# Performance work log

Measured on AMD Instinct MI355X. Metric: run time of the kernel, lower is better.

## Reference

```python
import jax, jax.numpy as jnp
import numpy as np

SIGMA_READ = 0.5
EPS = 1e-8

def setup_inputs() -> dict:
    key = jax.random.key(0)
    k1, k2, k3, k4, k5 = jax.random.split(key, 5)
    B, T, D = 2, 512, 128
    N, DV, DE = 100000, 256, 4
    q = jax.random.normal(k1, (B, T, D), dtype=jnp.float32)
    q = q / jnp.linalg.norm(q, axis=-1, keepdims=True)  # normalized queries
    K = jax.random.normal(k2, (N, D), dtype=jnp.float32)
    K = K / jnp.linalg.norm(K, axis=-1, keepdims=True)  # F.normalize(K, dim=-1)
    V = jax.random.normal(k3, (N, DV), dtype=jnp.float32)
    h = jax.random.uniform(k4, (N,), dtype=jnp.float32)  # intensities > 0
    e = jax.random.uniform(k5, (N, DE), dtype=jnp.float32)
    return {"queries": q, "K": K, "V": V, "h": h, "e": e, "top_k": 32}

def reference(queries, K, V, h, e, top_k):
    # similarities: [B, T, N]; all centers assumed active
    sim = jnp.einsum('btd,nd->btn', queries, K)
    dist_sq = 2.0 - 2.0 * sim
    rbf = jnp.exp(-dist_sq / (2.0 * SIGMA_READ ** 2))
    # top-k RBF weights and their center indices: [B, T, k]
    topk_w, topk_idx = jax.lax.top_k(rbf, top_k)
    h_topk = h[topk_idx]
    log_w = jnp.log(topk_w + EPS) + jnp.log(h_topk + EPS)
    weights = jax.nn.softmax(log_w, axis=-1)
    V_sel = V[topk_idx]  # [B, T, k, DV]
    e_sel = e[topk_idx]  # [B, T, k, DE]
    r_V = jnp.einsum('btk,btkv->btv', weights, V_sel)
    r_E = jnp.einsum('btk,btke->bte', weights, e_sel)
    return r_V, r_E, weights, topk_idx
```

## Files before the change

### kernel.cpp

```cpp
#include <hip/hip_runtime.h>
#include <math.h>


#define DDIM    128
#define MSAMPLE 12288
#define NBINS   256
#define TOPK    32
#define NQTOT   1024
#define NGRP    128
#define BCAP    24
#define EPSM    0.012f
#define SORTN   1024
#define FINEN   256
#define QSH     17
#define QMASK   0x1FFFFu
#define QMARGIN 200u

typedef __attribute__((ext_vector_type(8))) short short8;
typedef __attribute__((ext_vector_type(4))) float f32x4;

__device__ inline unsigned short f2bf(float f) {
    unsigned u = __builtin_bit_cast(unsigned, f);
    return (unsigned short)((u + 0x7FFFu + ((u >> 16) & 1u)) >> 16);
}

__global__ __launch_bounds__(256)
void convert_kernel(const float* __restrict__ Qg, const float* __restrict__ Kg,
                    unsigned short* __restrict__ Qbf, unsigned short* __restrict__ Kbf,
                    int nq8, int nk8)
{
    int total = nq8 + nk8;
    for (int i = blockIdx.x * 256 + threadIdx.x; i < total; i += gridDim.x * 256) {
        const float* s; unsigned short* d; int j;
        if (i < nq8) { s = Qg; d = Qbf; j = i; }
        else         { s = Kg; d = Kbf; j = i - nq8; }
        float4 a = *reinterpret_cast<const float4*>(s + (size_t)j * 8);
        float4 b = *reinterpret_cast<const float4*>(s + (size_t)j * 8 + 4);
        short8 o;
        o[0] = (short)f2bf(a.x); o[1] = (short)f2bf(a.y);
        o[2] = (short)f2bf(a.z); o[3] = (short)f2bf(a.w);
        o[4] = (short)f2bf(b.x); o[5] = (short)f2bf(b.y);
        o[6] = (short)f2bf(b.z); o[7] = (short)f2bf(b.w);
        *reinterpret_cast<short8*>(d + (size_t)j * 8) = o;
    }
}

template<int MODE>
__global__ __launch_bounds__(256)
void gemm_pass(const unsigned short* __restrict__ Qb, const unsigned short* __restrict__ Kb,
               int N, unsigned char* __restrict__ binsU8,
               const float* __restrict__ thr,
               int* __restrict__ cnt2, unsigned int* __restrict__ buckets)
{
    __shared__ __align__(16) unsigned char Bs[2][64 * 256];
    __shared__ int off_l[64];
    const int tid   = threadIdx.x;
    const int lane  = tid & 63;
    const int w     = tid >> 6;
    const int wr    = (w >> 1) * 32;
    const int wc    = (w & 1) * 32;
    const int lr    = lane & 15;
    const int lk    = lane >> 4;
    const int g     = blockIdx.x;
    const int qbase = blockIdx.y * 64;

    int t0, tcnt;
    if (MODE == 0) { t0 = g; tcnt = 1; }
    else { t0 = g * 12 + min(g, 27); tcnt = 12 + (g < 27 ? 1 : 0); }

    if (MODE == 1)
        for (int i = tid; i < 64; i += 256) off_l[i] = 0;

#define STAGE(buf, tile) do {                                                  \
    const int cbase_ = (tile) * 64;                                            \
    _Pragma("unroll")                                                          \
    for (int it = 0; it < 4; ++it) {                                           \
        int flat = it * 256 + tid;                                             \
        int r_ = flat >> 4, cc_ = flat & 15;                                   \
        int row_ = cbase_ + r_;                                                \
        if (MODE == 1 && row_ >= N) row_ = N - 1;   \
        const unsigned short* src_ = Kb + (size_t)row_ * DDIM                  \
                                        + ((cc_ ^ (r_ & 15)) * 8);             \
        unsigned char* dst_ = &Bs[buf][(size_t)(it * 256 + (tid & ~63)) * 16]; \
        __builtin_amdgcn_global_load_lds(                                      \
            (const __attribute__((address_space(1))) unsigned int*)src_,       \
            (__attribute__((address_space(3))) unsigned int*)dst_, 16, 0, 0);  \
    }                                                                          \
} while (0)

    short8 af[2][4];
    #pragma unroll
    for (int fm = 0; fm < 2; ++fm)
        #pragma unroll
        for (int ks = 0; ks < 4; ++ks)
            af[fm][ks] = *reinterpret_cast<const short8*>(
                Qb + (size_t)(qbase + wr + fm * 16 + lr) * DDIM + (ks * 4 + lk) * 8);

    float thrv[2][4];
    if (MODE == 1) {
        #pragma unroll
        for (int fm = 0; fm < 2; ++fm)
            #pragma unroll
            for (int j = 0; j < 4; ++j)
                thrv[fm][j] = thr[qbase + wr + fm * 16 + lk * 4 + j] - EPSM;
    }

    STAGE(0, t0);
    __syncthreads();
    int cur = 0;

    for (int t = 0; t < tcnt; ++t) {
        if (t + 1 < tcnt) STAGE(cur ^ 1, t0 + t + 1);

        const int cbase = (t0 + t) * 64;
        const unsigned char* bsc = Bs[cur];

        const f32x4 z = {0.f, 0.f, 0.f, 0.f};
        f32x4 acc[2][2];
        #pragma unroll
        for (int a = 0; a < 2; ++a)
            #pragma unroll
            for (int b = 0; b < 2; ++b) acc[a][b] = z;

        #pragma unroll
        for (int ks = 0; ks < 4; ++ks) {
            short8 bg[2];
            #pragma unroll
            for (int fn = 0; fn < 2; ++fn) {
                int rb = wc + fn * 16 + lr;
                bg[fn] = *reinterpret_cast<const short8*>(
                    bsc + rb * 256 + (((ks * 4 + lk) ^ (rb & 15)) << 4));
            }
            #pragma unroll
            for (int fm = 0; fm < 2; ++fm)
                #pragma unroll
                for (int fn = 0; fn < 2; ++fn)
                    acc[fm][fn] = __builtin_amdgcn_mfma_f32_16x16x32_bf16(
                        af[fm][ks], bg[fn], acc[fm][fn], 0, 0, 0);
        }

        #pragma unroll
        for (int fm = 0; fm < 2; ++fm) {
            #pragma unroll
            for (int j = 0; j < 4; ++j) {
                const int ql = wr + fm * 16 + lk * 4 + j;
                if (MODE == 0) {
                    #pragma unroll
                    for (int fn = 0; fn < 2; ++fn) {
                        const int c = cbase + wc + fn * 16 + lr;
                        float s = acc[fm][fn][j];
                        int b = (int)((s + 1.0f) * (NBINS * 0.5f));
                        b = b < 0 ? 0 : (b > NBINS - 1 ? NBINS - 1 : b);
                        binsU8[(size_t)(qbase + ql) * MSAMPLE + c] = (unsigned char)b;
                    }
                } else {
                    const float t_ = thrv[fm][j];
                    const float s0 = acc[fm][0][j], s1 = acc[fm][1][j];
                    if (__any(fmaxf(s0, s1) >= t_)) {
                        #pragma unroll
                        for (int fn = 0; fn < 2; ++fn) {
                            const int c = cbase + wc + fn * 16 + lr;
                            const float s = fn ? s1 : s0;
                            if (c < N && s >= t_) {
                                int qs = (int)((s + 1.0f) * 16384.0f);
                                qs = qs < 0 ? 0 : (qs > 32767 ? 32767 : qs);
                                unsigned key = ((unsigned)qs << QSH)
                                             | (~(unsigned)c & QMASK);
                                int p = atomicAdd(&off_l[ql], 1);
                                if (p < BCAP)
                                    buckets[((size_t)(qbase + ql) * NGRP + g) * BCAP + p] = key;
                            }
                        }
                    }
                }
            }
        }
        __syncthreads();
        cur ^= 1;
    }
#undef STAGE

    if (MODE == 1) {
        for (int i = tid; i < 64; i += 256)
            cnt2[(qbase + i) * NGRP + g] = min(off_l[i], BCAP);
    }
}

__global__ __launch_bounds__(256)
void thresh_kernel(const unsigned char* __restrict__ bins, float* __restrict__ thr)
{
    __shared__ int hS[4 * NBINS];
    __shared__ int hA[NBINS];
    __shared__ int hB[NBINS];
    __shared__ int best;
    const int q = blockIdx.x, tid = threadIdx.x;
    const int wv = tid >> 6;
    for (int i = tid; i < 4 * NBINS; i += 256) hS[i] = 0;
    if (tid == 0) best = 0;
    __syncthreads();
    const uint4* bp = reinterpret_cast<const uint4*>(bins + (size_t)q * MSAMPLE);
    int* hw = hS + wv * NBINS;
    for (int i = tid; i < MSAMPLE / 16; i += 256) {
        uint4 v = bp[i];
        unsigned xs[4] = {v.x, v.y, v.z, v.w};
        #pragma unroll
        for (int k = 0; k < 4; ++k) {
            unsigned x = xs[k];
            atomicAdd(&hw[x & 255], 1); x >>= 8;
            atomicAdd(&hw[x & 255], 1); x >>= 8;
            atomicAdd(&hw[x & 255], 1); x >>= 8;
            atomicAdd(&hw[x & 255], 1);
        }
    }
    __syncthreads();
    for (int i = tid; i < NBINS; i += 256)
        hA[i] = hS[i] + hS[NBINS + i] + hS[2 * NBINS + i] + hS[3 * NBINS + i];
    __syncthreads();
    int* src = hA; int* dst = hB;
    for (int off = 1; off < NBINS; off <<= 1) {
        for (int i = tid; i < NBINS; i += 256)
            dst[i] = src[i] + ((i + off < NBINS) ? src[i + off] : 0);
        __syncthreads();
        int* tmp = src; src = dst; dst = tmp;
    }
    for (int i = tid; i < NBINS; i += 256)
        if (src[i] >= TOPK) atomicMax(&best, i);
    __syncthreads();
    if (tid == 0)
        thr[q] = (float)(best - 1) * (2.0f / NBINS) - 1.0f;
}

__global__ __launch_bounds__(256)
void finalize_kernel(const unsigned int* __restrict__ buckets, const int* __restrict__ cnt2,
                     const float* __restrict__ Qg, const float* __restrict__ Kg,
                     const float* __restrict__ V, const float* __restrict__ hIn,
                     const float* __restrict__ eIn,
                     float* __restrict__ out, int N)
{
    __shared__ float qv[DDIM];
    __shared__ unsigned sk[SORTN];
    __shared__ unsigned fk[FINEN];
    __shared__ unsigned long long sk64[FINEN];
    __shared__ int hA[NBINS];
    __shared__ int hB[NBINS];
    __shared__ int cnts[NGRP], offs[NGRP];
    __shared__ int wpart[2];
    __shared__ int bestb, nsel;
    __shared__ float selV[TOPK];
    __shared__ int   selI[TOPK];
    __shared__ float wts[TOPK];
    const int q = blockIdx.x, tid = threadIdx.x;

    if (tid < DDIM) qv[tid] = Qg[(size_t)q * DDIM + tid];
    if (tid < NGRP) cnts[tid] = cnt2[q * NGRP + tid];
    for (int i = tid; i < SORTN; i += 256) sk[i] = 0u;
    if (tid < NBINS) hA[tid] = 0;
    if (tid < FINEN) sk64[tid] = 0ull;
    if (tid == 0) { bestb = 0; nsel = 0; }
    __syncthreads();
    int cv = 0, xv = 0;
    if (tid < NGRP) {
        cv = cnts[tid];
        xv = cv;
        #pragma unroll
        for (int o = 1; o < 64; o <<= 1) {
            int y = __shfl_up(xv, o);
            if ((tid & 63) >= o) xv += y;
        }
        if ((tid & 63) == 63) wpart[tid >> 6] = xv;
    }
    __syncthreads();
    if (tid < NGRP) {
        int add = (tid >= 64) ? wpart[0] : 0;
        offs[tid] = xv - cv + add;
    }
    __syncthreads();
    for (int flat = tid; flat < NGRP * BCAP; flat += 256) {
        int gg = flat / BCAP, j = flat - gg * BCAP;
        if (j < cnts[gg]) {
            int dst = offs[gg] + j;
            if (dst < SORTN)
                sk[dst] = buckets[((size_t)q * NGRP + gg) * BCAP + j];
        }
    }
    __syncthreads();
    for (int i = tid; i < SORTN; i += 256) {
        unsigned k = sk[i];
        if (k) atomicAdd(&hA[k >> 24], 1);
    }
    __syncthreads();
    {
        int* src = hA; int* dst = hB;
        for (int off = 1; off < NBINS; off <<= 1) {
            for (int i = tid; i < NBINS; i += 256)
                dst[i] = src[i] + ((i + off < NBINS) ? src[i + off] : 0);
            __syncthreads();
            int* tmp = src; src = dst; dst = tmp;
        }
        for (int i = tid; i < NBINS; i += 256)
            if (src[i] >= TOPK) atomicMax(&bestb, i);
    }
    __syncthreads();
    const unsigned b32q = (unsigned)bestb << 7;
    const unsigned cutq = b32q > QMARGIN ? b32q - QMARGIN : 0u;
    const unsigned cutKey = cutq << QSH;
    for (int i = tid; i < SORTN; i += 256) {
        unsigned k = sk[i];
        if (k != 0u && k >= cutKey) {
            int p = atomicAdd(&nsel, 1);
            if (p < FINEN) fk[p] = k;
        }
    }
    __syncthreads();
    const int m = min(nsel, FINEN);
    const int sub = tid & 3, ci = tid >> 2;
    #pragma unroll
    for (int base = 0; base < FINEN; base += 64) {
        int i = base + ci;
        bool act = i < m;
        int c = 0;
        float s = 0.f;
        if (act) {
            c = (int)(~fk[i] & QMASK);
            const float4* k4 = reinterpret_cast<const float4*>(Kg + (size_t)c * DDIM) + sub;
            const float4* q4 = reinterpret_cast<const float4*>(qv) + sub;
            #pragma unroll
            for (int d = 0; d < 8; ++d) {
                float4 kk = k4[d * 4];
                float4 qq = q4[d * 4];
                s = fmaf(qq.x, kk.x, s); s = fmaf(qq.y, kk.y, s);
                s = fmaf(qq.z, kk.z, s); s = fmaf(qq.w, kk.w, s);
            }
        }
        s += __shfl_xor(s, 1); s += __shfl_xor(s, 2);
        if (act && sub == 0) {
            float dist = 2.0f - 2.0f * s;
            float rbf = expf(dist * -2.0f);
            sk64[i] = ((unsigned long long)__float_as_uint(rbf) << 32)
                    | (unsigned)(~(unsigned)c);
        }
    }
    __syncthreads();
    for (int k = 2; k <= FINEN; k <<= 1) {
        for (int j = k >> 1; j > 0; j >>= 1) {
            int x = tid ^ j;
            if (x > tid) {
                unsigned long long a = sk64[tid], b = sk64[x];
                bool sw = ((tid & k) == 0) ? (a < b) : (a > b);
                if (sw) { sk64[tid] = b; sk64[x] = a; }
            }
            __syncthreads();
        }
    }
    if (tid < TOPK) {
        unsigned long long kk = sk64[tid];
        float rbf = __uint_as_float((unsigned)(kk >> 32));
        int   idx = (int)(~(unsigned)kk);
        selV[tid] = rbf; selI[tid] = idx;
        float lw = logf(rbf + 1e-8f) + logf(hIn[idx] + 1e-8f);
        float mx = lw;
        #pragma unroll
        for (int o = 16; o > 0; o >>= 1) mx = fmaxf(mx, __shfl_xor(mx, o));
        float ex = expf(lw - mx);
        float sm = ex;
        #pragma unroll
        for (int o = 16; o > 0; o >>= 1) sm += __shfl_xor(sm, o);
        wts[tid] = ex / sm;
    }
    __syncthreads();
    {
        float acc = 0.f;
        const int v = tid;
        #pragma unroll
        for (int k = 0; k < TOPK; ++k)
            acc = fmaf(wts[k], V[(size_t)selI[k] * 256 + v], acc);
        out[(size_t)q * 256 + v] = acc;
    }
    const int offE = NQTOT * 256;
    const int offW = offE + NQTOT * 4;
    const int offI = offW + NQTOT * TOPK;
    if (tid < 4) {
        float acc = 0.f;
        #pragma unroll
        for (int k = 0; k < TOPK; ++k)
            acc = fmaf(wts[k], eIn[(size_t)selI[k] * 4 + tid], acc);
        out[offE + q * 4 + tid] = acc;
    }
    if (tid < TOPK) {
        out[offW + q * TOPK + tid] = wts[tid];
        out[offI + q * TOPK + tid] = (float)selI[tid];
    }
}

extern "C" void kernel_launch(void* const* d_in, const int* in_sizes, int n_in,
                              void* d_out, int out_size, void* d_ws, size_t ws_size,
                              hipStream_t stream)
{
    (void)n_in; (void)out_size; (void)ws_size;
    const float* Qg = (const float*)d_in[0];
    const float* Kg = (const float*)d_in[1];
    const float* Vg = (const float*)d_in[2];
    const float* hg = (const float*)d_in[3];
    const float* eg = (const float*)d_in[4];
    const int N = in_sizes[1] / DDIM;

    char* w = (char*)d_ws;
    unsigned short* Kbf = (unsigned short*)w;  w += (size_t)N * DDIM * 2;
    unsigned short* Qbf = (unsigned short*)w;  w += (size_t)NQTOT * DDIM * 2;
    float* thr = (float*)w;                    w += NQTOT * 4;
    int*   cnt2 = (int*)w;                     w += (size_t)NQTOT * NGRP * 4;
    unsigned char* binsU8 = (unsigned char*)w;
    unsigned int*  buckets = (unsigned int*)w;

    hipMemsetAsync(cnt2, 0, (size_t)NQTOT * NGRP * 4, stream);

    dim3 blk(256);
    convert_kernel<<<dim3(2048), blk, 0, stream>>>(
        Qg, Kg, Qbf, Kbf, NQTOT * DDIM / 8, N * DDIM / 8);
    gemm_pass<0><<<dim3(MSAMPLE / 64, NQTOT / 64), blk, 0, stream>>>(
        Qbf, Kbf, N, binsU8, nullptr, nullptr, nullptr);
    thresh_kernel<<<dim3(NQTOT), blk, 0, stream>>>(binsU8, thr);
    gemm_pass<1><<<dim3(NGRP, NQTOT / 64), blk, 0, stream>>>(
        Qbf, Kbf, N, nullptr, thr, cnt2, buckets);
    finalize_kernel<<<dim3(NQTOT), blk, 0, stream>>>(
        buckets, cnt2, Qg, Kg, Vg, hg, eg, (float*)d_out, N);
}
```

Before: 131.2 us.

## Stage K tiles in half-depth chunks to halve LDS double-buffer footprint

The K tile staging is split along the feature dimension into two 64-wide halves, so each LDS buffer holds half a tile (16KB total instead of 32KB). Each tile now runs two MFMA phases, with the second-half load issued during the first phase and the next tile's first half issued during the second. The aim is a smaller LDS footprint, allowing more resident blocks per CU, plus finer-grained overlap of loads with compute. The cost is an extra barrier and buffer swap per tile and shorter compute phases for hiding each load.

```diff
diff --git a/kernel.cpp b/kernel.cpp
--- a/kernel.cpp
+++ b/kernel.cpp
@@ -52,7 +52,7 @@
                const float* __restrict__ thr,
                int* __restrict__ cnt2, unsigned int* __restrict__ buckets)
 {
-    __shared__ __align__(16) unsigned char Bs[2][64 * 256];
+    __shared__ __align__(16) unsigned char Bs[2][64 * 128];
     __shared__ int off_l[64];
     const int tid   = threadIdx.x;
     const int lane  = tid & 63;
@@ -71,16 +71,16 @@
     if (MODE == 1)
         for (int i = tid; i < 64; i += 256) off_l[i] = 0;
 
-#define STAGE(buf, tile) do {                                                  \
+#define STAGE(buf, tile, half) do {                                            \
     const int cbase_ = (tile) * 64;                                            \
     _Pragma("unroll")                                                          \
-    for (int it = 0; it < 4; ++it) {                                           \
-        int flat = it * 256 + tid;                                             \
-        int r_ = flat >> 4, cc_ = flat & 15;                                   \
+    for (int it = 0; it < 2; ++it) {                                           \
+        int flat = it * 256 + tid;                                 \
+        int r_ = flat >> 3, cc_ = flat & 7;         \
         int row_ = cbase_ + r_;                                                \
         if (MODE == 1 && row_ >= N) row_ = N - 1;   \
-        const unsigned short* src_ = Kb + (size_t)row_ * DDIM                  \
-                                        + ((cc_ ^ (r_ & 15)) * 8);             \
+        const unsigned short* src_ = Kb + (size_t)row_ * DDIM + (half) * 64    \
+                                        + ((cc_ ^ (r_ & 7)) * 8);              \
         unsigned char* dst_ = &Bs[buf][(size_t)(it * 256 + (tid & ~63)) * 16]; \
         __builtin_amdgcn_global_load_lds(                                      \
             (const __attribute__((address_space(1))) unsigned int*)src_,       \
@@ -105,15 +105,12 @@
                 thrv[fm][j] = thr[qbase + wr + fm * 16 + lk * 4 + j] - EPSM;
     }
 
-    STAGE(0, t0);
+    STAGE(0, t0, 0);
     __syncthreads();
     int cur = 0;
 
     for (int t = 0; t < tcnt; ++t) {
-        if (t + 1 < tcnt) STAGE(cur ^ 1, t0 + t + 1);
-
         const int cbase = (t0 + t) * 64;
-        const unsigned char* bsc = Bs[cur];
 
         const f32x4 z = {0.f, 0.f, 0.f, 0.f};
         f32x4 acc[2][2];
@@ -122,21 +119,48 @@
             #pragma unroll
             for (int b = 0; b < 2; ++b) acc[a][b] = z;
 
-        #pragma unroll
-        for (int ks = 0; ks < 4; ++ks) {
-            short8 bg[2];
-            #pragma unroll
-            for (int fn = 0; fn < 2; ++fn) {
-                int rb = wc + fn * 16 + lr;
-                bg[fn] = *reinterpret_cast<const short8*>(
-                    bsc + rb * 256 + (((ks * 4 + lk) ^ (rb & 15)) << 4));
+        STAGE(cur ^ 1, t0 + t, 1);
+        {
+            const unsigned char* bsc = Bs[cur];
+            #pragma unroll
+            for (int ksl = 0; ksl < 2; ++ksl) {
+                short8 bg[2];
+                #pragma unroll
+                for (int fn = 0; fn < 2; ++fn) {
+                    int rb = wc + fn * 16 + lr;
+                    bg[fn] = *reinterpret_cast<const short8*>(
+                        bsc + rb * 128 + (((ksl * 4 + lk) ^ (rb & 7)) << 4));
+                }
+                #pragma unroll
+                for (int fm = 0; fm < 2; ++fm)
+                    #pragma unroll
+                    for (int fn = 0; fn < 2; ++fn)
+                        acc[fm][fn] = __builtin_amdgcn_mfma_f32_16x16x32_bf16(
+                            af[fm][ksl], bg[fn], acc[fm][fn], 0, 0, 0);
             }
-            #pragma unroll
-            for (int fm = 0; fm < 2; ++fm)
+        }
+        __syncthreads();
+        cur ^= 1;
+
+        if (t + 1 < tcnt) STAGE(cur ^ 1, t0 + t + 1, 0);
+        {
+            const unsigned char* bsc = Bs[cur];
+            #pragma unroll
+            for (int ksl = 0; ksl < 2; ++ksl) {
+                short8 bg[2];
                 #pragma unroll
-                for (int fn = 0; fn < 2; ++fn)
-                    acc[fm][fn] = __builtin_amdgcn_mfma_f32_16x16x32_bf16(
-                        af[fm][ks], bg[fn], acc[fm][fn], 0, 0, 0);
+                for (int fn = 0; fn < 2; ++fn) {
+                    int rb = wc + fn * 16 + lr;
+                    bg[fn] = *reinterpret_cast<const short8*>(
+                        bsc + rb * 128 + (((ksl * 4 + lk) ^ (rb & 7)) << 4));
+                }
+                #pragma unroll
+                for (int fm = 0; fm < 2; ++fm)
+                    #pragma unroll
+                    for (int fn = 0; fn < 2; ++fn)
+                        acc[fm][fn] = __builtin_amdgcn_mfma_f32_16x16x32_bf16(
+                            af[fm][2 + ksl], bg[fn], acc[fm][fn], 0, 0, 0);
+            }
         }
 
         #pragma unroll
```

Measured after the change: 131.5 us. About the same (+0.2%).

## Replace LDS-staged GEMM tiles with per-wave register-loaded K over 1024-key ranges

Applied to the files above, without the earlier changes.

The similarity passes drop the shared-memory double-buffered K staging. Each wave now handles its own 32 queries and loads K fragments straight from global memory into registers, with a two-tile software pipeline. Each block now covers 128 queries and a contiguous range of 1024 keys, and the candidate pass uses 104 groups (98 active) instead of 128. This removes LDS traffic and block-wide barriers, at the cost of every wave reloading the same K data through cache and using more registers.

```diff
diff --git a/kernel.cpp b/kernel.cpp
--- a/kernel.cpp
+++ b/kernel.cpp
@@ -7,7 +7,8 @@
 #define NBINS   256
 #define TOPK    32
 #define NQTOT   1024
-#define NGRP    128
+#define NGRP    104
+#define NRANGE  98
 #define BCAP    24
 #define EPSM    0.012f
 #define SORTN   1024
@@ -47,46 +48,23 @@
 
 template<int MODE>
 __global__ __launch_bounds__(256)
-void gemm_pass(const unsigned short* __restrict__ Qb, const unsigned short* __restrict__ Kb,
-               int N, unsigned char* __restrict__ binsU8,
-               const float* __restrict__ thr,
-               int* __restrict__ cnt2, unsigned int* __restrict__ buckets)
+void sim_pass(const unsigned short* __restrict__ Qb, const unsigned short* __restrict__ Kb,
+              int N, unsigned char* __restrict__ binsU8,
+              const float* __restrict__ thr,
+              int* __restrict__ cnt2, unsigned int* __restrict__ buckets)
 {
-    __shared__ __align__(16) unsigned char Bs[2][64 * 256];
-    __shared__ int off_l[64];
-    const int tid   = threadIdx.x;
-    const int lane  = tid & 63;
-    const int w     = tid >> 6;
-    const int wr    = (w >> 1) * 32;
-    const int wc    = (w & 1) * 32;
-    const int lr    = lane & 15;
-    const int lk    = lane >> 4;
-    const int g     = blockIdx.x;
-    const int qbase = blockIdx.y * 64;
-
-    int t0, tcnt;
-    if (MODE == 0) { t0 = g; tcnt = 1; }
-    else { t0 = g * 12 + min(g, 27); tcnt = 12 + (g < 27 ? 1 : 0); }
-
-    if (MODE == 1)
-        for (int i = tid; i < 64; i += 256) off_l[i] = 0;
-
-#define STAGE(buf, tile) do {                                                  \
-    const int cbase_ = (tile) * 64;                                            \
-    _Pragma("unroll")                                                          \
-    for (int it = 0; it < 4; ++it) {                                           \
-        int flat = it * 256 + tid;                                             \
-        int r_ = flat >> 4, cc_ = flat & 15;                                   \
-        int row_ = cbase_ + r_;                                                \
-        if (MODE == 1 && row_ >= N) row_ = N - 1;   \
-        const unsigned short* src_ = Kb + (size_t)row_ * DDIM                  \
-                                        + ((cc_ ^ (r_ & 15)) * 8);             \
-        unsigned char* dst_ = &Bs[buf][(size_t)(it * 256 + (tid & ~63)) * 16]; \
-        __builtin_amdgcn_global_load_lds(                                      \
-            (const __attribute__((address_space(1))) unsigned int*)src_,       \
-            (__attribute__((address_space(3))) unsigned int*)dst_, 16, 0, 0);  \
-    }                                                                          \
-} while (0)
+    __shared__ int off_l[128];
+    const int tid  = threadIdx.x;
+    const int lane = tid & 63;
+    const int w    = tid >> 6;
+    const int lr   = lane & 15;
+    const int lk   = lane >> 4;
+    const int r    = blockIdx.x;
+    const int qbase = blockIdx.y * 128 + w * 32;
+    const int rangeBase = r * 1024;
+
+    if (MODE == 1 && rangeBase >= N) return;
+    const bool safe = (rangeBase + 1024) <= N;
 
     short8 af[2][4];
     #pragma unroll
@@ -94,7 +72,7 @@
         #pragma unroll
         for (int ks = 0; ks < 4; ++ks)
             af[fm][ks] = *reinterpret_cast<const short8*>(
-                Qb + (size_t)(qbase + wr + fm * 16 + lr) * DDIM + (ks * 4 + lk) * 8);
+                Qb + (size_t)(qbase + fm * 16 + lr) * DDIM + (ks * 4 + lk) * 8);
 
     float thrv[2][4];
     if (MODE == 1) {
@@ -102,87 +80,105 @@
         for (int fm = 0; fm < 2; ++fm)
             #pragma unroll
             for (int j = 0; j < 4; ++j)
-                thrv[fm][j] = thr[qbase + wr + fm * 16 + lk * 4 + j] - EPSM;
-    }
-
-    STAGE(0, t0);
-    __syncthreads();
-    int cur = 0;
-
-    for (int t = 0; t < tcnt; ++t) {
-        if (t + 1 < tcnt) STAGE(cur ^ 1, t0 + t + 1);
-
-        const int cbase = (t0 + t) * 64;
-        const unsigned char* bsc = Bs[cur];
-
-        const f32x4 z = {0.f, 0.f, 0.f, 0.f};
-        f32x4 acc[2][2];
-        #pragma unroll
-        for (int a = 0; a < 2; ++a)
-            #pragma unroll
-            for (int b = 0; b < 2; ++b) acc[a][b] = z;
-
-        #pragma unroll
-        for (int ks = 0; ks < 4; ++ks) {
-            short8 bg[2];
-            #pragma unroll
-            for (int fn = 0; fn < 2; ++fn) {
-                int rb = wc + fn * 16 + lr;
-                bg[fn] = *reinterpret_cast<const short8*>(
-                    bsc + rb * 256 + (((ks * 4 + lk) ^ (rb & 15)) << 4));
-            }
-            #pragma unroll
-            for (int fm = 0; fm < 2; ++fm)
-                #pragma unroll
-                for (int fn = 0; fn < 2; ++fn)
-                    acc[fm][fn] = __builtin_amdgcn_mfma_f32_16x16x32_bf16(
-                        af[fm][ks], bg[fn], acc[fm][fn], 0, 0, 0);
-        }
-
-        #pragma unroll
-        for (int fm = 0; fm < 2; ++fm) {
-            #pragma unroll
-            for (int j = 0; j < 4; ++j) {
-                const int ql = wr + fm * 16 + lk * 4 + j;
-                if (MODE == 0) {
-                    #pragma unroll
-                    for (int fn = 0; fn < 2; ++fn) {
-                        const int c = cbase + wc + fn * 16 + lr;
-                        float s = acc[fm][fn][j];
-                        int b = (int)((s + 1.0f) * (NBINS * 0.5f));
-                        b = b < 0 ? 0 : (b > NBINS - 1 ? NBINS - 1 : b);
-                        binsU8[(size_t)(qbase + ql) * MSAMPLE + c] = (unsigned char)b;
-                    }
-                } else {
-                    const float t_ = thrv[fm][j];
-                    const float s0 = acc[fm][0][j], s1 = acc[fm][1][j];
-                    if (__any(fmaxf(s0, s1) >= t_)) {
-                        #pragma unroll
-                        for (int fn = 0; fn < 2; ++fn) {
-                            const int c = cbase + wc + fn * 16 + lr;
-                            const float s = fn ? s1 : s0;
-                            if (c < N && s >= t_) {
-                                int qs = (int)((s + 1.0f) * 16384.0f);
-                                qs = qs < 0 ? 0 : (qs > 32767 ? 32767 : qs);
-                                unsigned key = ((unsigned)qs << QSH)
-                                             | (~(unsigned)c & QMASK);
-                                int p = atomicAdd(&off_l[ql], 1);
-                                if (p < BCAP)
-                                    buckets[((size_t)(qbase + ql) * NGRP + g) * BCAP + p] = key;
-                            }
-                        }
-                    }
-                }
-            }
-        }
-        __syncthreads();
-        cur ^= 1;
-    }
-#undef STAGE
+                thrv[fm][j] = thr[qbase + fm * 16 + lk * 4 + j] - EPSM;
+        if (lane < 32) off_l[w * 32 + lane] = 0;
+    }
+
+#define LOADBG(dst, tt) do {                                                   \
+    const int cb_ = rangeBase + (tt) * 32;                                     \
+    if (safe) {                                                                \
+        _Pragma("unroll")                                                      \
+        for (int fn_ = 0; fn_ < 2; ++fn_)                                      \
+            _Pragma("unroll")                                                  \
+            for (int ks_ = 0; ks_ < 4; ++ks_)                                  \
+                dst[fn_][ks_] = *reinterpret_cast<const short8*>(              \
+                    Kb + (size_t)(cb_ + fn_ * 16 + lr) * DDIM                  \
+                       + (ks_ * 4 + lk) * 8);                                  \
+    } else {                                                                   \
+        _Pragma("unroll")                                                      \
+        for (int fn_ = 0; fn_ < 2; ++fn_)                                      \
+            _Pragma("unroll")                                                  \
+            for (int ks_ = 0; ks_ < 4; ++ks_) {                                \
+                int row_ = cb_ + fn_ * 16 + lr;                                \
+                if (row_ >= N) row_ = N - 1;        \
+                dst[fn_][ks_] = *reinterpret_cast<const short8*>(              \
+                    Kb + (size_t)row_ * DDIM + (ks_ * 4 + lk) * 8);            \
+            }                                                                  \
+    }                                                                          \
+} while (0)
+
+#define COMPUTE(bgX, tt) do {                                                  \
+    const int cbase_ = rangeBase + (tt) * 32;                                  \
+    const f32x4 z_ = {0.f, 0.f, 0.f, 0.f};                                     \
+    f32x4 acc[2][2];                                                           \
+    _Pragma("unroll")                                                          \
+    for (int a_ = 0; a_ < 2; ++a_)                                             \
+        _Pragma("unroll")                                                      \
+        for (int b_ = 0; b_ < 2; ++b_) acc[a_][b_] = z_;                       \
+    _Pragma("unroll")                                                          \
+    for (int ks_ = 0; ks_ < 4; ++ks_)                                          \
+        _Pragma("unroll")                                                      \
+        for (int fm_ = 0; fm_ < 2; ++fm_)                                      \
+            _Pragma("unroll")                                                  \
+            for (int fn_ = 0; fn_ < 2; ++fn_)                                  \
+                acc[fm_][fn_] = __builtin_amdgcn_mfma_f32_16x16x32_bf16(       \
+                    af[fm_][ks_], bgX[fn_][ks_], acc[fm_][fn_], 0, 0, 0);      \
+     \
+    _Pragma("unroll")                                                          \
+    for (int fm_ = 0; fm_ < 2; ++fm_) {                                        \
+        _Pragma("unroll")                                                      \
+        for (int j_ = 0; j_ < 4; ++j_) {                                       \
+            const int qlw = fm_ * 16 + lk * 4 + j_;     \
+            if (MODE == 0) {                                                   \
+                _Pragma("unroll")                                              \
+                for (int fn_ = 0; fn_ < 2; ++fn_) {                            \
+                    const int c_ = cbase_ + fn_ * 16 + lr;                     \
+                    float s_ = acc[fm_][fn_][j_];                              \
+                    int b_ = (int)((s_ + 1.0f) * (NBINS * 0.5f));              \
+                    b_ = b_ < 0 ? 0 : (b_ > NBINS - 1 ? NBINS - 1 : b_);       \
+                    binsU8[(size_t)(qbase + qlw) * MSAMPLE + c_] =             \
+                        (unsigned char)b_;                                     \
+                }                                                              \
+            } else {                                                           \
+                const float t_ = thrv[fm_][j_];                                \
+                const float s0_ = acc[fm_][0][j_], s1_ = acc[fm_][1][j_];      \
+                if (__any(fmaxf(s0_, s1_) >= t_)) {                            \
+                    _Pragma("unroll")                                          \
+                    for (int fn_ = 0; fn_ < 2; ++fn_) {                        \
+                        const int c_ = cbase_ + fn_ * 16 + lr;                 \
+                        const float s_ = fn_ ? s1_ : s0_;                      \
+                        if (c_ < N && s_ >= t_) {                              \
+                            int qs_ = (int)((s_ + 1.0f) * 16384.0f);           \
+                            qs_ = qs_ < 0 ? 0 : (qs_ > 32767 ? 32767 : qs_);   \
+                            unsigned key_ = ((unsigned)qs_ << QSH)             \
+                                          | (~(unsigned)c_ & QMASK);           \
+                            int p_ = atomicAdd(&off_l[w * 32 + qlw], 1);       \
+                            if (p_ < BCAP)                                     \
+                                buckets[((size_t)(qbase + qlw) * NGRP + r)     \
+                                        * BCAP + p_] = key_;                   \
+                        }                                                      \
+                    }                                                          \
+                }                                                              \
+            }                                                                  \
+        }                                                                      \
+    }                                                                          \
+} while (0)
+
+    short8 bgA[2][4], bgB[2][4];
+    LOADBG(bgA, 0);
+    for (int t = 0; t < 32; t += 2) {
+        LOADBG(bgB, t + 1);
+        COMPUTE(bgA, t);
+        if (t + 2 < 32) LOADBG(bgA, t + 2);
+        COMPUTE(bgB, t + 1);
+    }
+#undef LOADBG
+#undef COMPUTE
 
     if (MODE == 1) {
-        for (int i = tid; i < 64; i += 256)
-            cnt2[(qbase + i) * NGRP + g] = min(off_l[i], BCAP);
+        if (lane < 32)
+            cnt2[(size_t)(qbase + lane) * NGRP + r] =
+                min(off_l[w * 32 + lane], BCAP);
     }
 }
 
@@ -417,10 +413,10 @@
     dim3 blk(256);
     convert_kernel<<<dim3(2048), blk, 0, stream>>>(
         Qg, Kg, Qbf, Kbf, NQTOT * DDIM / 8, N * DDIM / 8);
-    gemm_pass<0><<<dim3(MSAMPLE / 64, NQTOT / 64), blk, 0, stream>>>(
+    sim_pass<0><<<dim3(MSAMPLE / 1024, NQTOT / 128), blk, 0, stream>>>(
         Qbf, Kbf, N, binsU8, nullptr, nullptr, nullptr);
     thresh_kernel<<<dim3(NQTOT), blk, 0, stream>>>(binsU8, thr);
-    gemm_pass<1><<<dim3(NGRP, NQTOT / 64), blk, 0, stream>>>(
+    sim_pass<1><<<dim3(NGRP, NQTOT / 128), blk, 0, stream>>>(
         Qbf, Kbf, N, nullptr, thr, cnt2, buckets);
     finalize_kernel<<<dim3(NQTOT), blk, 0, stream>>>(
         buckets, cnt2, Qg, Kg, Vg, hg, eg, (float*)d_out, N);
```

Result: slower. 229.5 us (+74.9%).
